# Performance work log

Measured on AMD Instinct MI355X. Metric: run time of the kernel, lower is better.

Reference implementation:

```python
import jax, jax.numpy as jnp
import numpy as np

N = 100000        # nodes
E = 1600000       # edges (no self loops)
NFEAT = 512
NHEADS = 3
NH1 = 8           # per-head out dim of layer 1 -> x1 has 24 cols
D1 = NHEADS * NH1
NCLASS = 32
LRELU = 0.2


def _seg_sum(vals, idx, n=N):
    return jax.ops.segment_sum(vals, idx, num_segments=n)


def _spmm(idx, vals, x):
    # sparse [N,N] @ dense [N,F]: out[i] = sum_{e: row=i} vals[e] * x[col[e]]
    return _seg_sum(vals[:, None] * x[idx[1]], idx[0])


def _relation(ft, nb, g1, g2, b1, b2, r):
    gamma = jax.nn.leaky_relu(ft @ g1 + nb @ g2, LRELU) + 1.0
    beta = jax.nn.leaky_relu(ft @ b1 + nb @ b2, LRELU)
    return ft + gamma * r + beta - nb          # transE-style m


def _gat_head(h, a, src, dst):
    # h: [N, out], a: [2*out]; edge-wise unnormalized attention then scatter-agg
    z = jnp.concatenate([h[src], h[dst]], axis=1) @ a          # [E']
    ee = jnp.exp(-jax.nn.leaky_relu(z, LRELU))                 # [E']
    rowsum = _seg_sum(ee, src)                                 # [N]
    hp = _seg_sum(ee[:, None] * h[dst], src) / rowsum[:, None] # [N, out]
    return jax.nn.elu(hp)                                      # concat=True path


def setup_inputs() -> dict:
    key = jax.random.key(0)
    ks = jax.random.split(key, 20)
    s = 0.05

    def w(k, shape):
        return jax.random.normal(k, shape, jnp.float32) * s

    x = jax.random.normal(ks[0], (N, NFEAT), jnp.float32)
    adj_indices = jax.random.randint(ks[1], (2, E), 0, N, dtype=jnp.int32)
    adj_values = jax.random.uniform(ks[2], (E,), jnp.float32)
    es = jax.random.randint(ks[3], (2, E + N), 0, N, dtype=jnp.int32)
    loops = jnp.arange(N, dtype=jnp.int32)
    adj_self_indices = es.at[:, E:].set(jnp.stack([loops, loops]))  # ensure self loops

    return {
        "x": x,
        "adj_values": adj_values,
        "w_g1": w(ks[4], (NFEAT, NFEAT)), "w_g2": w(ks[5], (NFEAT, NFEAT)),
        "w_b1": w(ks[6], (NFEAT, NFEAT)), "w_b2": w(ks[7], (NFEAT, NFEAT)),
        "r1_r": w(ks[8], (NFEAT,)),
        "gat1_W": w(ks[9], (NHEADS, NFEAT, NH1)),
        "gat1_a": w(ks[10], (NHEADS, 2 * NH1)),
        "w2_g1": w(ks[11], (D1, D1)), "w2_g2": w(ks[12], (D1, D1)),
        "w2_b1": w(ks[13], (D1, D1)), "w2_b2": w(ks[14], (D1, D1)),
        "r2_r": w(ks[15], (D1,)),
        "gat2_W": w(ks[16], (D1, NCLASS)),
        "gat2_a": w(ks[17], (2 * NCLASS,)),
        "adj_indices": adj_indices,
        "adj_self_indices": adj_self_indices,
        "head": 0,
    }


def reference(x, adj_values, w_g1, w_g2, w_b1, w_b2, r1_r, gat1_W, gat1_a,
              w2_g1, w2_g2, w2_b1, w2_b2, r2_r, gat2_W, gat2_a,
              adj_indices, adj_self_indices, head):
    src, dst = adj_self_indices[0], adj_self_indices[1]

    # ---- layer 1 (TailGAT_SP body), eval mode (dropout = identity) ----
    neighbor = _spmm(adj_indices, adj_values, x)
    m1 = _relation(x, neighbor, w_g1, w_g2, w_b1, w_b2, r1_r)
    hin = x if head else x + m1          # mi injected when not head (ablation=0)
    h = jnp.einsum('nf,hfo->hno', hin, gat1_W)                  # [3, N, 8]
    x1 = jax.vmap(lambda hh, aa: _gat_head(hh, aa, src, dst))(h, gat1_a)
    x1 = jnp.transpose(x1, (1, 0, 2)).reshape(N, D1)            # torch.cat(dim=1)
    x1 = jax.nn.elu(x1)

    # ---- layer 2 (TransGAT_SP, nheads=1) ----
    neighbor2 = _spmm(adj_indices, adj_values, x1)
    m2 = _relation(x1, neighbor2, w2_g1, w2_g2, w2_b1, w2_b2, r2_r)
    hin2 = x1 if head else x1 + m2
    x2 = _gat_head(hin2 @ gat2_W, gat2_a, src, dst)             # [N, nclass]

    return x2, jnp.linalg.norm(m1, axis=1), jnp.linalg.norm(m2, axis=1)
```

## Files before the change

### kernel.cpp

```cpp
#include <hip/hip_runtime.h>
#include <stdint.h>

typedef __bf16 bf16;
typedef __bf16 bf16x8 __attribute__((ext_vector_type(8)));
typedef float  f32x4  __attribute__((ext_vector_type(4)));

#define LRELU_S 0.2f

__device__ __forceinline__ float lrelu(float v){ return v > 0.f ? v : LRELU_S * v; }
__device__ __forceinline__ float eluf(float v){ return v > 0.f ? v : expm1f(v); }

__global__ void k_count(const int* __restrict__ adj, const int* __restrict__ selfe,
                        unsigned* __restrict__ cnt1, unsigned* __restrict__ cnt2, int E, int EN){
  int i = blockIdx.x * blockDim.x + threadIdx.x;
  if (i < E)  atomicAdd(&cnt1[adj[i]], 1u);
  if (i < EN) atomicAdd(&cnt2[selfe[i]], 1u);
}

__global__ void k_scan(unsigned* __restrict__ cnt, unsigned* __restrict__ rp, int n){
  __shared__ unsigned s[1024];
  int t = threadIdx.x;
  int chunk = (n + 1023) >> 10;
  int lo = t * chunk, hi = lo + chunk;
  if (lo > n) lo = n;
  if (hi > n) hi = n;
  unsigned sum = 0;
  for (int i = lo; i < hi; i++) sum += cnt[i];
  s[t] = sum; __syncthreads();
  for (int d = 1; d < 1024; d <<= 1){
    unsigned add = (t >= d) ? s[t - d] : 0u;
    __syncthreads();
    s[t] += add;
    __syncthreads();
  }
  unsigned run = s[t] - sum;
  for (int i = lo; i < hi; i++){ rp[i] = run; run += cnt[i]; cnt[i] = 0u; }
  if (hi == n) rp[n] = run;
}

__global__ void k_fill(const int* __restrict__ adj, const int* __restrict__ selfe,
                       const float* __restrict__ avals,
                       const unsigned* __restrict__ rp1, const unsigned* __restrict__ rp2,
                       unsigned* __restrict__ cur1, unsigned* __restrict__ cur2,
                       int* __restrict__ cols1, float* __restrict__ vals1,
                       int* __restrict__ dst2, int E, int EN){
  int i = blockIdx.x * blockDim.x + threadIdx.x;
  if (i < E){
    int r = adj[i];
    unsigned slot = rp1[r] + atomicAdd(&cur1[r], 1u);
    cols1[slot] = adj[E + i];
    vals1[slot] = avals[i];
  }
  if (i < EN){
    int sN = selfe[i];
    unsigned slot = rp2[sN] + atomicAdd(&cur2[sN], 1u);
    dst2[slot] = selfe[EN + i];
  }
}

__global__ void k_cvt_x(const float* __restrict__ x, bf16* __restrict__ xb, int n8){
  int i = blockIdx.x * blockDim.x + threadIdx.x;
  if (i >= n8) return;
  const f32x4* p = (const f32x4*)(x + (size_t)i * 8);
  f32x4 a = p[0], b = p[1];
  bf16x8 o;
  o[0]=(bf16)a[0]; o[1]=(bf16)a[1]; o[2]=(bf16)a[2]; o[3]=(bf16)a[3];
  o[4]=(bf16)b[0]; o[5]=(bf16)b[1]; o[6]=(bf16)b[2]; o[7]=(bf16)b[3];
  *(bf16x8*)(xb + (size_t)i * 8) = o;
}

__global__ void k_build_wt(const float* __restrict__ wg1, const float* __restrict__ wg2,
                           const float* __restrict__ wb1, const float* __restrict__ wb2,
                           bf16* __restrict__ Wt){
  int i = blockIdx.x * blockDim.x + threadIdx.x;
  int c = i >> 10, k = i & 1023;
  float v;
  if (c < 512) v = (k < 512) ? wg1[k * 512 + c] : wg2[(k - 512) * 512 + c];
  else { int cc = c - 512; v = (k < 512) ? wb1[k * 512 + cc] : wb2[(k - 512) * 512 + cc]; }
  Wt[(size_t)c * 1024 + k] = (bf16)v;
}

__global__ void k_build_w1b(const float* __restrict__ g1W, bf16* __restrict__ g1Wb){
  int i = blockIdx.x * blockDim.x + threadIdx.x;
  if (i >= 32 * 512) return;
  int c = i >> 9, k = i & 511;
  float v = 0.f;
  if (c < 24){ int h = c >> 3, o = c & 7; v = g1W[h * 4096 + k * 8 + o]; }
  g1Wb[i] = (bf16)v;
}

__global__ __launch_bounds__(256) void k_spmm1(const unsigned* __restrict__ rp, const int* __restrict__ cols,
    const float* __restrict__ vals, const bf16* __restrict__ xb, bf16* __restrict__ nbb, int N){
  int lane = threadIdx.x & 63;
  int r = blockIdx.x * 4 + (threadIdx.x >> 6);
  if (r >= N) return;
  unsigned b0 = rp[r], b1 = rp[r + 1];
  float acc[8] = {0.f,0.f,0.f,0.f,0.f,0.f,0.f,0.f};
  unsigned e = b0;
  for (; e + 4 <= b1; e += 4){
    int c0 = cols[e], c1 = cols[e+1], c2 = cols[e+2], c3 = cols[e+3];
    float v0 = vals[e], v1 = vals[e+1], v2 = vals[e+2], v3 = vals[e+3];
    bf16x8 x0 = *(const bf16x8*)(xb + (size_t)c0 * 512 + lane * 8);
    bf16x8 x1 = *(const bf16x8*)(xb + (size_t)c1 * 512 + lane * 8);
    bf16x8 x2 = *(const bf16x8*)(xb + (size_t)c2 * 512 + lane * 8);
    bf16x8 x3 = *(const bf16x8*)(xb + (size_t)c3 * 512 + lane * 8);
    #pragma unroll
    for (int j = 0; j < 8; j++)
      acc[j] += v0 * (float)x0[j] + v1 * (float)x1[j] + v2 * (float)x2[j] + v3 * (float)x3[j];
  }
  for (; e < b1; ++e){
    int c = cols[e]; float v = vals[e];
    bf16x8 xv = *(const bf16x8*)(xb + (size_t)c * 512 + lane * 8);
    #pragma unroll
    for (int j = 0; j < 8; j++) acc[j] += v * (float)xv[j];
  }
  bf16x8 o;
  #pragma unroll
  for (int j = 0; j < 8; j++) o[j] = (bf16)acc[j];
  *(bf16x8*)(nbb + (size_t)r * 512 + lane * 8) = o;
}

__global__ __launch_bounds__(256) void k_gemm1f(const bf16* __restrict__ xb, const bf16* __restrict__ nbb,
    const bf16* __restrict__ Wt, const float* __restrict__ r1, const int* __restrict__ headp,
    bf16* __restrict__ hinb, float* __restrict__ nrmsq, int M){
  __shared__ __align__(16) bf16 As[2][128 * 32];
  __shared__ __align__(16) bf16 Bg[2][128 * 32];
  __shared__ __align__(16) bf16 Bb[2][128 * 32];
  int bid = blockIdx.x;
  int chunk = gridDim.x >> 3;
  int tile = (bid & 7) * chunk + (bid >> 3);
  int rowBase = (tile >> 2) * 128;
  int fBase = (tile & 3) * 128;
  int tid = threadIdx.x, wave = tid >> 6, lane = tid & 63;
  int wm = wave >> 1, wn = wave & 1;
  f32x4 aG[4][4], aB[4][4];
  #pragma unroll
  for (int m = 0; m < 4; m++)
    #pragma unroll
    for (int n = 0; n < 4; n++){ aG[m][n] = (f32x4){0.f,0.f,0.f,0.f}; aB[m][n] = (f32x4){0.f,0.f,0.f,0.f}; }

  int sRow = wave * 16 + (lane >> 2);
  int sColSwz = (((lane & 3) ^ ((lane >> 3) & 3))) * 8;

  auto stage = [&](int buf, int kt){
    const bf16* Abase = (kt < 16) ? xb : nbb;
    int kcol = (kt & 15) * 32;
    #pragma unroll
    for (int c = 0; c < 2; c++){
      int rr = c * 64 + sRow;
      int grow = rowBase + rr; if (grow >= M) grow = M - 1;
      const bf16* asrc = Abase + (size_t)grow * 512 + kcol + sColSwz;
      __builtin_amdgcn_global_load_lds((const __attribute__((address_space(1))) void*)asrc,
          (__attribute__((address_space(3))) void*)&As[buf][(size_t)(c * 64 + wave * 16) * 32], 16, 0, 0);
      const bf16* gsrc = Wt + (size_t)(fBase + rr) * 1024 + kt * 32 + sColSwz;
      __builtin_amdgcn_global_load_lds((const __attribute__((address_space(1))) void*)gsrc,
          (__attribute__((address_space(3))) void*)&Bg[buf][(size_t)(c * 64 + wave * 16) * 32], 16, 0, 0);
      const bf16* bsrc = Wt + (size_t)(512 + fBase + rr) * 1024 + kt * 32 + sColSwz;
      __builtin_amdgcn_global_load_lds((const __attribute__((address_space(1))) void*)bsrc,
          (__attribute__((address_space(3))) void*)&Bb[buf][(size_t)(c * 64 + wave * 16) * 32], 16, 0, 0);
    }
  };

  stage(0, 0);
  __syncthreads();
  int cur = 0;
  int fr = lane & 15;
  int sRead = (((lane >> 4) ^ ((fr >> 1) & 3))) * 8;
  for (int kt = 0; kt < 32; ++kt){
    if (kt + 1 < 32) stage(cur ^ 1, kt + 1);
    bf16x8 af[4], bg[4], bb[4];
    #pragma unroll
    for (int m = 0; m < 4; m++)
      af[m] = *(const bf16x8*)&As[cur][(wm * 64 + m * 16 + fr) * 32 + sRead];
    #pragma unroll
    for (int n = 0; n < 4; n++){
      bg[n] = *(const bf16x8*)&Bg[cur][(wn * 64 + n * 16 + fr) * 32 + sRead];
      bb[n] = *(const bf16x8*)&Bb[cur][(wn * 64 + n * 16 + fr) * 32 + sRead];
    }
    #pragma unroll
    for (int m = 0; m < 4; m++)
      #pragma unroll
      for (int n = 0; n < 4; n++){
        aG[m][n] = __builtin_amdgcn_mfma_f32_16x16x32_bf16(af[m], bg[n], aG[m][n], 0, 0, 0);
        aB[m][n] = __builtin_amdgcn_mfma_f32_16x16x32_bf16(af[m], bb[n], aB[m][n], 0, 0, 0);
      }
    __syncthreads();
    cur ^= 1;
  }

  int head = *headp;
  float rf[4];
  #pragma unroll
  for (int n = 0; n < 4; n++) rf[n] = r1[fBase + wn * 64 + n * 16 + (lane & 15)];
  #pragma unroll
  for (int m = 0; m < 4; m++){
    #pragma unroll
    for (int j = 0; j < 4; j++){
      int row = rowBase + wm * 64 + m * 16 + (lane >> 4) * 4 + j;
      bool ok = row < M;
      int rowc = ok ? row : M - 1;
      float msq = 0.f;
      #pragma unroll
      for (int n = 0; n < 4; n++){
        int f = fBase + wn * 64 + n * 16 + (lane & 15);
        float g = lrelu(aG[m][n][j]);
        float b = lrelu(aB[m][n][j]);
        float xf = (float)xb[(size_t)rowc * 512 + f];
        float nf = (float)nbb[(size_t)rowc * 512 + f];
        float mv = xf + (g + 1.f) * rf[n] + b - nf;
        msq += mv * mv;
        float hin = head ? xf : (xf + mv);
        if (ok) hinb[(size_t)row * 512 + f] = (bf16)hin;
      }
      #pragma unroll
      for (int d = 1; d < 16; d <<= 1) msq += __shfl_xor(msq, d);
      if (ok && (lane & 15) == 0) atomicAdd(&nrmsq[row], msq);
    }
  }
}

__global__ __launch_bounds__(256) void k_proj1(const bf16* __restrict__ hinb, const bf16* __restrict__ g1Wb,
    float* __restrict__ h1, int N){
  __shared__ __align__(16) bf16 Bs[32 * 520];
  __shared__ __align__(16) bf16 As[256 * 32];
  int tid = threadIdx.x, wave = tid >> 6, lane = tid & 63;
  #pragma unroll
  for (int i = 0; i < 8; i++){
    int e8 = tid + i * 256;
    int c = e8 >> 6, k = (e8 & 63) * 8;
    bf16x8 v = *(const bf16x8*)(g1Wb + c * 512 + k);
    *(bf16x8*)&Bs[c * 520 + k] = v;
  }
  int rBase = blockIdx.x * 256;
  f32x4 acc[4][2];
  #pragma unroll
  for (int m = 0; m < 4; m++){ acc[m][0] = (f32x4){0,0,0,0}; acc[m][1] = (f32x4){0,0,0,0}; }
  __syncthreads();
  for (int kt = 0; kt < 16; ++kt){
    #pragma unroll
    for (int i = 0; i < 4; i++){
      int r = (tid >> 2) + i * 64;
      int grow = rBase + r; if (grow >= N) grow = N - 1;
      const bf16* src = hinb + (size_t)grow * 512 + kt * 32 + (tid & 3) * 8;
      __builtin_amdgcn_global_load_lds((const __attribute__((address_space(1))) void*)src,
          (__attribute__((address_space(3))) void*)&As[(size_t)(i * 64 + wave * 16) * 32], 16, 0, 0);
    }
    __syncthreads();
    bf16x8 bf0 = *(const bf16x8*)&Bs[(0 * 16 + (lane & 15)) * 520 + kt * 32 + (lane >> 4) * 8];
    bf16x8 bf1 = *(const bf16x8*)&Bs[(1 * 16 + (lane & 15)) * 520 + kt * 32 + (lane >> 4) * 8];
    #pragma unroll
    for (int m = 0; m < 4; m++){
      bf16x8 af = *(const bf16x8*)&As[(wave * 64 + m * 16 + (lane & 15)) * 32 + (lane >> 4) * 8];
      acc[m][0] = __builtin_amdgcn_mfma_f32_16x16x32_bf16(af, bf0, acc[m][0], 0, 0, 0);
      acc[m][1] = __builtin_amdgcn_mfma_f32_16x16x32_bf16(af, bf1, acc[m][1], 0, 0, 0);
    }
    __syncthreads();
  }
  #pragma unroll
  for (int m = 0; m < 4; m++)
    #pragma unroll
    for (int n = 0; n < 2; n++)
      #pragma unroll
      for (int j = 0; j < 4; j++){
        int row = rBase + wave * 64 + m * 16 + (lane >> 4) * 4 + j;
        int col = n * 16 + (lane & 15);
        if (row < N) h1[(size_t)row * 32 + col] = acc[m][n][j];
      }
}

__global__ __launch_bounds__(256) void k_att1(const float* __restrict__ h1, const float* __restrict__ g1a,
    const float* __restrict__ nrmsq, float* __restrict__ a1s, float* __restrict__ a1d,
    float* __restrict__ nrm1, int N){
  int lane = threadIdx.x & 63;
  int r = blockIdx.x * 4 + (threadIdx.x >> 6);
  if (r >= N) return;
  if (lane < 24){
    float hv = h1[(size_t)r * 32 + lane];
    int h = lane >> 3, o = lane & 7;
    float ps = hv * g1a[h * 16 + o];
    float pd = hv * g1a[h * 16 + 8 + o];
    #pragma unroll
    for (int d = 1; d < 8; d <<= 1){ ps += __shfl_xor(ps, d); pd += __shfl_xor(pd, d); }
    if (o == 0){ a1s[r * 4 + h] = ps; a1d[r * 4 + h] = pd; }
  } else if (lane == 24){
    nrm1[r] = sqrtf(nrmsq[r]);
  }
}

__global__ __launch_bounds__(256) void k_gat1(const unsigned* __restrict__ rp2, const int* __restrict__ dst2,
    const float* __restrict__ h1, const float* __restrict__ a1s, const float* __restrict__ a1d,
    float* __restrict__ x1, int N){
  int lane = threadIdx.x & 63;
  int r = blockIdx.x * 8 + (threadIdx.x >> 6) * 2 + (lane >> 5);
  if (r >= N) return;
  int l2 = lane & 31;
  int cl = (l2 < 24) ? l2 : 0;
  int h = cl >> 3;
  float as = a1s[r * 4 + h];
  unsigned b0 = rp2[r], b1 = rp2[r + 1];
  float hp = 0.f, rs = 0.f;
  for (unsigned e = b0; e < b1; ++e){
    int d = dst2[e];
    float z = as + a1d[d * 4 + h];
    float ee = expf(-lrelu(z));
    hp += ee * h1[(size_t)d * 32 + cl];
    rs += ee;
  }
  if (l2 < 24){
    float v = hp / rs;
    v = eluf(v); v = eluf(v);
    x1[(size_t)r * 24 + l2] = v;
  }
}

__global__ __launch_bounds__(256) void k_spmm2(const unsigned* __restrict__ rp, const int* __restrict__ cols,
    const float* __restrict__ vals, const float* __restrict__ x1, float* __restrict__ nb2, int N){
  int lane = threadIdx.x & 63;
  int r = blockIdx.x * 8 + (threadIdx.x >> 6) * 2 + (lane >> 5);
  if (r >= N) return;
  int l2 = lane & 31;
  int cl = (l2 < 24) ? l2 : 0;
  unsigned b0 = rp[r], b1 = rp[r + 1];
  float acc = 0.f;
  for (unsigned e = b0; e < b1; ++e)
    acc += vals[e] * x1[(size_t)cols[e] * 24 + cl];
  if (l2 < 24) nb2[(size_t)r * 24 + l2] = acc;
}

__global__ void k_rel2(const float* __restrict__ x1, const float* __restrict__ nb2,
    const float* __restrict__ wg1, const float* __restrict__ wg2,
    const float* __restrict__ wb1, const float* __restrict__ wb2,
    const float* __restrict__ r2, const float* __restrict__ W2, const float* __restrict__ a2,
    const int* __restrict__ headp,
    float* __restrict__ hg, float* __restrict__ a2s, float* __restrict__ a2d,
    float* __restrict__ nrm2, int N){
  int r = blockIdx.x * blockDim.x + threadIdx.x;
  if (r >= N) return;
  int head = *headp;
  float xr[24], nr[24], hin[24];
  #pragma unroll
  for (int i = 0; i < 24; i++){ xr[i] = x1[(size_t)r*24+i]; nr[i] = nb2[(size_t)r*24+i]; }
  float nrm = 0.f;
  #pragma unroll
  for (int j = 0; j < 24; j++){
    float gp = 0.f, bp = 0.f;
    #pragma unroll
    for (int i = 0; i < 24; i++){
      gp += xr[i] * wg1[i*24+j] + nr[i] * wg2[i*24+j];
      bp += xr[i] * wb1[i*24+j] + nr[i] * wb2[i*24+j];
    }
    float m = xr[j] + (lrelu(gp) + 1.f) * r2[j] + lrelu(bp) - nr[j];
    nrm += m * m;
    hin[j] = head ? xr[j] : (xr[j] + m);
  }
  nrm2[r] = sqrtf(nrm);
  float as = 0.f, ad = 0.f;
  #pragma unroll
  for (int c = 0; c < 32; c++){
    float v = 0.f;
    #pragma unroll
    for (int i = 0; i < 24; i++) v += hin[i] * W2[i*32+c];
    hg[(size_t)r*32 + c] = v;
    as += v * a2[c]; ad += v * a2[32 + c];
  }
  a2s[r] = as; a2d[r] = ad;
}

__global__ __launch_bounds__(256) void k_gat2(const unsigned* __restrict__ rp2, const int* __restrict__ dst2,
    const float* __restrict__ hg, const float* __restrict__ a2s, const float* __restrict__ a2d,
    float* __restrict__ out, int N){
  int lane = threadIdx.x & 63;
  int r = blockIdx.x * 8 + (threadIdx.x >> 6) * 2 + (lane >> 5);
  if (r >= N) return;
  int cl = lane & 31;
  float as = a2s[r];
  unsigned b0 = rp2[r], b1 = rp2[r + 1];
  float hp = 0.f, rs = 0.f;
  for (unsigned e = b0; e < b1; ++e){
    int d = dst2[e];
    float z = as + a2d[d];
    float ee = expf(-lrelu(z));
    hp += ee * hg[(size_t)d * 32 + cl];
    rs += ee;
  }
  out[(size_t)r * 32 + cl] = eluf(hp / rs);
}

extern "C" void kernel_launch(void* const* d_in, const int* in_sizes, int n_in,
                              void* d_out, int out_size, void* d_ws, size_t ws_size,
                              hipStream_t stream){
  const float* x     = (const float*)d_in[0];
  const float* avals = (const float*)d_in[1];
  const float* wg1   = (const float*)d_in[2];
  const float* wg2   = (const float*)d_in[3];
  const float* wb1   = (const float*)d_in[4];
  const float* wb2   = (const float*)d_in[5];
  const float* r1    = (const float*)d_in[6];
  const float* g1W   = (const float*)d_in[7];
  const float* g1a   = (const float*)d_in[8];
  const float* w2g1  = (const float*)d_in[9];
  const float* w2g2  = (const float*)d_in[10];
  const float* w2b1  = (const float*)d_in[11];
  const float* w2b2  = (const float*)d_in[12];
  const float* r2    = (const float*)d_in[13];
  const float* W2    = (const float*)d_in[14];
  const float* a2    = (const float*)d_in[15];
  const int*   adj   = (const int*)d_in[16];
  const int*   selfe = (const int*)d_in[17];
  const int*   headp = (const int*)d_in[18];

  const int N  = in_sizes[0] / 512;
  const int E  = in_sizes[1];
  const int EN = in_sizes[17] / 2;

  char* w = (char*)d_ws; size_t off = 0;
  auto carve = [&](size_t bytes) -> char* {
    char* p = w + off; off = (off + bytes + 255) & ~(size_t)255; return p;
  };
  unsigned* rp1   = (unsigned*)carve(((size_t)N + 1) * 4);
  unsigned* rp2   = (unsigned*)carve(((size_t)N + 1) * 4);
  unsigned* cnt1  = (unsigned*)carve(((size_t)N + 1) * 4);
  unsigned* cnt2  = (unsigned*)carve(((size_t)N + 1) * 4);
  int*      cols1 = (int*)carve((size_t)E * 4);
  float*    vals1 = (float*)carve((size_t)E * 4);
  int*      dst2  = (int*)carve((size_t)EN * 4);
  bf16*     xb    = (bf16*)carve((size_t)N * 512 * 2);
  bf16*     nbb   = (bf16*)carve((size_t)N * 512 * 2);
  bf16*     Wt    = (bf16*)carve((size_t)1024 * 1024 * 2);
  bf16*     g1Wb  = (bf16*)carve((size_t)32 * 512 * 2);
  bf16*     hinb  = (bf16*)carve((size_t)N * 512 * 2);
  float*    nrmsq = (float*)carve((size_t)N * 4);
  float*    h1    = (float*)carve((size_t)N * 32 * 4);
  float*    a1s   = (float*)carve((size_t)N * 4 * 4);
  float*    a1d   = (float*)carve((size_t)N * 4 * 4);
  float*    x1    = (float*)carve((size_t)N * 24 * 4);
  float*    nb2   = (float*)carve((size_t)N * 24 * 4);
  float*    hg    = (float*)carve((size_t)N * 32 * 4);
  float*    a2s   = (float*)carve((size_t)N * 4);
  float*    a2d   = (float*)carve((size_t)N * 4);

  float* out  = (float*)d_out;
  float* nrm1 = out + (size_t)N * 32;
  float* nrm2 = nrm1 + N;

  hipMemsetAsync(cnt1, 0, ((size_t)N + 1) * 4, stream);
  hipMemsetAsync(cnt2, 0, ((size_t)N + 1) * 4, stream);
  hipMemsetAsync(nrmsq, 0, (size_t)N * 4, stream);

  const int tb = 256;
  k_count<<<(EN + tb - 1) / tb, tb, 0, stream>>>(adj, selfe, cnt1, cnt2, E, EN);
  k_scan<<<1, 1024, 0, stream>>>(cnt1, rp1, N);
  k_scan<<<1, 1024, 0, stream>>>(cnt2, rp2, N);
  k_fill<<<(EN + tb - 1) / tb, tb, 0, stream>>>(adj, selfe, avals, rp1, rp2, cnt1, cnt2,
                                                cols1, vals1, dst2, E, EN);
  int n8 = N * 512 / 8;
  k_cvt_x<<<(n8 + tb - 1) / tb, tb, 0, stream>>>(x, xb, n8);
  k_build_wt<<<(1024 * 1024) / tb, tb, 0, stream>>>(wg1, wg2, wb1, wb2, Wt);
  k_build_w1b<<<(32 * 512) / tb, tb, 0, stream>>>(g1W, g1Wb);

  int rb = (N + 3) / 4;
  int rb8 = (N + 7) / 8;
  k_spmm1<<<rb, 256, 0, stream>>>(rp1, cols1, vals1, xb, nbb, N);

  int rowTiles = (N + 127) / 128;
  k_gemm1f<<<rowTiles * 4, 256, 0, stream>>>(xb, nbb, Wt, r1, headp, hinb, nrmsq, N);

  int pb = (N + 255) / 256;
  k_proj1<<<pb, 256, 0, stream>>>(hinb, g1Wb, h1, N);
  k_att1<<<rb, 256, 0, stream>>>(h1, g1a, nrmsq, a1s, a1d, nrm1, N);
  k_gat1<<<rb8, 256, 0, stream>>>(rp2, dst2, h1, a1s, a1d, x1, N);
  k_spmm2<<<rb8, 256, 0, stream>>>(rp1, cols1, vals1, x1, nb2, N);
  k_rel2<<<(N + tb - 1) / tb, tb, 0, stream>>>(x1, nb2, w2g1, w2g2, w2b1, w2b2, r2, W2, a2,
                                               headp, hg, a2s, a2d, nrm2, N);
  k_gat2<<<rb8, 256, 0, stream>>>(rp2, dst2, hg, a2s, a2d, out, N);
}
```

Measured before the change: 2.358 ms.

## Triple-buffer gemm1 with explicit waitcnt and store GAT features in bf16

The relation GEMM moves from two to three LDS buffers and prefetches two k-tiles ahead. Explicit vmcnt waits and raw barriers replace __syncthreads, so loads can stay in flight across iterations. Separately, the layer-1 and layer-2 GAT features (h1, x1, hg) are stored in bf16, and the per-head destination attention term is packed into the spare columns of each h1 row. This cuts the bytes touched by the edge gathers in gat1, spmm2 and gat2, at the cost of more LDS per block (which may lower occupancy) and reduced precision on intermediate activations.

```diff
diff --git a/kernel.cpp b/kernel.cpp
--- a/kernel.cpp
+++ b/kernel.cpp
@@ -123,9 +123,9 @@
 __global__ __launch_bounds__(256) void k_gemm1f(const bf16* __restrict__ xb, const bf16* __restrict__ nbb,
     const bf16* __restrict__ Wt, const float* __restrict__ r1, const int* __restrict__ headp,
     bf16* __restrict__ hinb, float* __restrict__ nrmsq, int M){
-  __shared__ __align__(16) bf16 As[2][128 * 32];
-  __shared__ __align__(16) bf16 Bg[2][128 * 32];
-  __shared__ __align__(16) bf16 Bb[2][128 * 32];
+  __shared__ __align__(16) bf16 As[3][128 * 32];
+  __shared__ __align__(16) bf16 Bg[3][128 * 32];
+  __shared__ __align__(16) bf16 Bb[3][128 * 32];
   int bid = blockIdx.x;
   int chunk = gridDim.x >> 3;
   int tile = (bid & 7) * chunk + (bid >> 3);
@@ -162,12 +162,18 @@
   };
 
   stage(0, 0);
-  __syncthreads();
+  stage(1, 1);
   int cur = 0;
   int fr = lane & 15;
   int sRead = (((lane >> 4) ^ ((fr >> 1) & 3))) * 8;
   for (int kt = 0; kt < 32; ++kt){
-    if (kt + 1 < 32) stage(cur ^ 1, kt + 1);
+    int nxt2 = cur + 2; if (nxt2 >= 3) nxt2 -= 3;
+    if (kt + 2 < 32) stage(nxt2, kt + 2);
+    if (kt < 30)       asm volatile("s_waitcnt vmcnt(12)" ::: "memory");
+    else if (kt == 30) asm volatile("s_waitcnt vmcnt(6)"  ::: "memory");
+    else               asm volatile("s_waitcnt vmcnt(0)"  ::: "memory");
+    __builtin_amdgcn_s_barrier();
+    __builtin_amdgcn_sched_barrier(0);
     bf16x8 af[4], bg[4], bb[4];
     #pragma unroll
     for (int m = 0; m < 4; m++)
@@ -184,8 +190,9 @@
         aG[m][n] = __builtin_amdgcn_mfma_f32_16x16x32_bf16(af[m], bg[n], aG[m][n], 0, 0, 0);
         aB[m][n] = __builtin_amdgcn_mfma_f32_16x16x32_bf16(af[m], bb[n], aB[m][n], 0, 0, 0);
       }
-    __syncthreads();
-    cur ^= 1;
+    asm volatile("s_waitcnt lgkmcnt(0)" ::: "memory");
+    __builtin_amdgcn_s_barrier();
+    cur = (cur + 1 == 3) ? 0 : cur + 1;
   }
 
   int head = *headp;
@@ -220,7 +227,7 @@
 }
 
 __global__ __launch_bounds__(256) void k_proj1(const bf16* __restrict__ hinb, const bf16* __restrict__ g1Wb,
-    float* __restrict__ h1, int N){
+    bf16* __restrict__ h1b, int N){
   __shared__ __align__(16) bf16 Bs[32 * 520];
   __shared__ __align__(16) bf16 As[256 * 32];
   int tid = threadIdx.x, wave = tid >> 6, lane = tid & 63;
@@ -264,32 +271,34 @@
       for (int j = 0; j < 4; j++){
         int row = rBase + wave * 64 + m * 16 + (lane >> 4) * 4 + j;
         int col = n * 16 + (lane & 15);
-        if (row < N) h1[(size_t)row * 32 + col] = acc[m][n][j];
+        if (row < N) h1b[(size_t)row * 32 + col] = (bf16)acc[m][n][j];
       }
 }
 
-__global__ __launch_bounds__(256) void k_att1(const float* __restrict__ h1, const float* __restrict__ g1a,
-    const float* __restrict__ nrmsq, float* __restrict__ a1s, float* __restrict__ a1d,
-    float* __restrict__ nrm1, int N){
+__global__ __launch_bounds__(256) void k_att1(bf16* __restrict__ h1b, const float* __restrict__ g1a,
+    const float* __restrict__ nrmsq, float* __restrict__ a1s, float* __restrict__ nrm1, int N){
   int lane = threadIdx.x & 63;
   int r = blockIdx.x * 4 + (threadIdx.x >> 6);
   if (r >= N) return;
   if (lane < 24){
-    float hv = h1[(size_t)r * 32 + lane];
+    float hv = (float)h1b[(size_t)r * 32 + lane];
     int h = lane >> 3, o = lane & 7;
     float ps = hv * g1a[h * 16 + o];
     float pd = hv * g1a[h * 16 + 8 + o];
     #pragma unroll
     for (int d = 1; d < 8; d <<= 1){ ps += __shfl_xor(ps, d); pd += __shfl_xor(pd, d); }
-    if (o == 0){ a1s[r * 4 + h] = ps; a1d[r * 4 + h] = pd; }
+    if (o == 0){
+      a1s[r * 4 + h] = ps;
+      h1b[(size_t)r * 32 + 24 + h] = (bf16)pd;
+    }
   } else if (lane == 24){
     nrm1[r] = sqrtf(nrmsq[r]);
   }
 }
 
 __global__ __launch_bounds__(256) void k_gat1(const unsigned* __restrict__ rp2, const int* __restrict__ dst2,
-    const float* __restrict__ h1, const float* __restrict__ a1s, const float* __restrict__ a1d,
-    float* __restrict__ x1, int N){
+    const bf16* __restrict__ h1b, const float* __restrict__ a1s,
+    bf16* __restrict__ x1b, int N){
   int lane = threadIdx.x & 63;
   int r = blockIdx.x * 8 + (threadIdx.x >> 6) * 2 + (lane >> 5);
   if (r >= N) return;
@@ -301,20 +310,22 @@
   float hp = 0.f, rs = 0.f;
   for (unsigned e = b0; e < b1; ++e){
     int d = dst2[e];
-    float z = as + a1d[d * 4 + h];
+    const bf16* rowp = h1b + (size_t)d * 32;
+    float ad = (float)rowp[24 + h];
+    float z = as + ad;
     float ee = expf(-lrelu(z));
-    hp += ee * h1[(size_t)d * 32 + cl];
+    hp += ee * (float)rowp[cl];
     rs += ee;
   }
   if (l2 < 24){
     float v = hp / rs;
     v = eluf(v); v = eluf(v);
-    x1[(size_t)r * 24 + l2] = v;
+    x1b[(size_t)r * 24 + l2] = (bf16)v;
   }
 }
 
 __global__ __launch_bounds__(256) void k_spmm2(const unsigned* __restrict__ rp, const int* __restrict__ cols,
-    const float* __restrict__ vals, const float* __restrict__ x1, float* __restrict__ nb2, int N){
+    const float* __restrict__ vals, const bf16* __restrict__ x1b, float* __restrict__ nb2, int N){
   int lane = threadIdx.x & 63;
   int r = blockIdx.x * 8 + (threadIdx.x >> 6) * 2 + (lane >> 5);
   if (r >= N) return;
@@ -323,23 +334,23 @@
   unsigned b0 = rp[r], b1 = rp[r + 1];
   float acc = 0.f;
   for (unsigned e = b0; e < b1; ++e)
-    acc += vals[e] * x1[(size_t)cols[e] * 24 + cl];
+    acc += vals[e] * (float)x1b[(size_t)cols[e] * 24 + cl];
   if (l2 < 24) nb2[(size_t)r * 24 + l2] = acc;
 }
 
-__global__ void k_rel2(const float* __restrict__ x1, const float* __restrict__ nb2,
+__global__ void k_rel2(const bf16* __restrict__ x1b, const float* __restrict__ nb2,
     const float* __restrict__ wg1, const float* __restrict__ wg2,
     const float* __restrict__ wb1, const float* __restrict__ wb2,
     const float* __restrict__ r2, const float* __restrict__ W2, const float* __restrict__ a2,
     const int* __restrict__ headp,
-    float* __restrict__ hg, float* __restrict__ a2s, float* __restrict__ a2d,
+    bf16* __restrict__ hgb, float* __restrict__ a2s, float* __restrict__ a2d,
     float* __restrict__ nrm2, int N){
   int r = blockIdx.x * blockDim.x + threadIdx.x;
   if (r >= N) return;
   int head = *headp;
   float xr[24], nr[24], hin[24];
   #pragma unroll
-  for (int i = 0; i < 24; i++){ xr[i] = x1[(size_t)r*24+i]; nr[i] = nb2[(size_t)r*24+i]; }
+  for (int i = 0; i < 24; i++){ xr[i] = (float)x1b[(size_t)r*24+i]; nr[i] = nb2[(size_t)r*24+i]; }
   float nrm = 0.f;
   #pragma unroll
   for (int j = 0; j < 24; j++){
@@ -360,14 +371,14 @@
     float v = 0.f;
     #pragma unroll
     for (int i = 0; i < 24; i++) v += hin[i] * W2[i*32+c];
-    hg[(size_t)r*32 + c] = v;
+    hgb[(size_t)r*32 + c] = (bf16)v;
     as += v * a2[c]; ad += v * a2[32 + c];
   }
   a2s[r] = as; a2d[r] = ad;
 }
 
 __global__ __launch_bounds__(256) void k_gat2(const unsigned* __restrict__ rp2, const int* __restrict__ dst2,
-    const float* __restrict__ hg, const float* __restrict__ a2s, const float* __restrict__ a2d,
+    const bf16* __restrict__ hgb, const float* __restrict__ a2s, const float* __restrict__ a2d,
     float* __restrict__ out, int N){
   int lane = threadIdx.x & 63;
   int r = blockIdx.x * 8 + (threadIdx.x >> 6) * 2 + (lane >> 5);
@@ -380,7 +391,7 @@
     int d = dst2[e];
     float z = as + a2d[d];
     float ee = expf(-lrelu(z));
-    hp += ee * hg[(size_t)d * 32 + cl];
+    hp += ee * (float)hgb[(size_t)d * 32 + cl];
     rs += ee;
   }
   out[(size_t)r * 32 + cl] = eluf(hp / rs);
@@ -430,12 +441,11 @@
   bf16*     g1Wb  = (bf16*)carve((size_t)32 * 512 * 2);
   bf16*     hinb  = (bf16*)carve((size_t)N * 512 * 2);
   float*    nrmsq = (float*)carve((size_t)N * 4);
-  float*    h1    = (float*)carve((size_t)N * 32 * 4);
+  bf16*     h1b   = (bf16*)carve((size_t)N * 32 * 2);
   float*    a1s   = (float*)carve((size_t)N * 4 * 4);
-  float*    a1d   = (float*)carve((size_t)N * 4 * 4);
-  float*    x1    = (float*)carve((size_t)N * 24 * 4);
+  bf16*     x1b   = (bf16*)carve((size_t)N * 24 * 2);
   float*    nb2   = (float*)carve((size_t)N * 24 * 4);
-  float*    hg    = (float*)carve((size_t)N * 32 * 4);
+  bf16*     hgb   = (bf16*)carve((size_t)N * 32 * 2);
   float*    a2s   = (float*)carve((size_t)N * 4);
   float*    a2d   = (float*)carve((size_t)N * 4);
 
@@ -466,11 +476,11 @@
   k_gemm1f<<<rowTiles * 4, 256, 0, stream>>>(xb, nbb, Wt, r1, headp, hinb, nrmsq, N);
 
   int pb = (N + 255) / 256;
-  k_proj1<<<pb, 256, 0, stream>>>(hinb, g1Wb, h1, N);
-  k_att1<<<rb, 256, 0, stream>>>(h1, g1a, nrmsq, a1s, a1d, nrm1, N);
-  k_gat1<<<rb8, 256, 0, stream>>>(rp2, dst2, h1, a1s, a1d, x1, N);
-  k_spmm2<<<rb8, 256, 0, stream>>>(rp1, cols1, vals1, x1, nb2, N);
-  k_rel2<<<(N + tb - 1) / tb, tb, 0, stream>>>(x1, nb2, w2g1, w2g2, w2b1, w2b2, r2, W2, a2,
-                                               headp, hg, a2s, a2d, nrm2, N);
-  k_gat2<<<rb8, 256, 0, stream>>>(rp2, dst2, hg, a2s, a2d, out, N);
-}
+  k_proj1<<<pb, 256, 0, stream>>>(hinb, g1Wb, h1b, N);
+  k_att1<<<rb, 256, 0, stream>>>(h1b, g1a, nrmsq, a1s, nrm1, N);
+  k_gat1<<<rb8, 256, 0, stream>>>(rp2, dst2, h1b, a1s, x1b, N);
+  k_spmm2<<<rb8, 256, 0, stream>>>(rp1, cols1, vals1, x1b, nb2, N);
+  k_rel2<<<(N + tb - 1) / tb, tb, 0, stream>>>(x1b, nb2, w2g1, w2g2, w2b1, w2b2, r2, W2, a2,
+                                               headp, hgb, a2s, a2d, nrm2, N);
+  k_gat2<<<rb8, 256, 0, stream>>>(rp2, dst2, hgb, a2s, a2d, out, N);
+}
```

New measurement: 2.512 ms. 6.6% more time.
